# Kernel tuning notes

Measured on AMD Instinct MI355X. Metric: run time of the kernel, lower is better.

The kernel has to match this reference:

```python
import jax, jax.numpy as jnp
import numpy as np

NUM_SUBSET = 3
BN_EPS = 1e-5


def setup_inputs() -> dict:
    key = jax.random.key(0)
    ks = jax.random.split(key, 6)
    N, C, T, V = 32, 192, 256, 25
    x = jax.random.normal(ks[0], (N, C, T, V), dtype=jnp.float32)
    w_in = jax.random.normal(ks[1], (3 * C, C), dtype=jnp.float32) * (1.0 / np.sqrt(C))
    b_in = jax.random.normal(ks[2], (3 * C,), dtype=jnp.float32) * 0.02
    w_ff = jax.random.normal(ks[3], (C, C), dtype=jnp.float32) * (1.0 / np.sqrt(C))
    b_ff = jax.random.normal(ks[4], (C,), dtype=jnp.float32) * 0.02
    bn_gamma = jnp.ones((C,), dtype=jnp.float32)
    bn_beta = jnp.zeros((C,), dtype=jnp.float32)
    bn_mean = jnp.zeros((C,), dtype=jnp.float32)
    bn_var = jnp.ones((C,), dtype=jnp.float32)
    return dict(x=x, w_in=w_in, b_in=b_in, w_ff=w_ff, b_ff=b_ff,
                bn_gamma=bn_gamma, bn_beta=bn_beta, bn_mean=bn_mean, bn_var=bn_var)


def reference(x, w_in, b_in, w_ff, b_ff, bn_gamma, bn_beta, bn_mean, bn_var):
    N, C, T, V = x.shape
    S = NUM_SUBSET
    mid = C // S
    # 1x1 conv QKV projection: (N,C,T,V) x (3C,C) -> (N,3C,T,V)
    qkv = jnp.einsum('nctv,dc->ndtv', x, w_in) + b_in[None, :, None, None]
    qkv = qkv.reshape(N, 3 * S, mid, T, V)
    q, k, v = jnp.split(qkv, 3, axis=1)  # each (N,S,mid,T,V)
    # tanh-normalized attention over time: (N,S,T,T)
    att = jnp.tanh(jnp.einsum('nsctv,nscqv->nstq', q, k) / (mid * V))
    y = jnp.einsum('nstq,nscqv->nsctv', att, v).reshape(N, C, T, V)
    # ff_nett: 1x1 conv + BatchNorm (inference form)
    y = jnp.einsum('nctv,dc->ndtv', y, w_ff) + b_ff[None, :, None, None]
    inv = bn_gamma / jnp.sqrt(bn_var + BN_EPS)
    y = (y - bn_mean[None, :, None, None]) * inv[None, :, None, None] + bn_beta[None, :, None, None]
    # residual + LeakyReLU(0.1)
    z = x + y
    return jnp.where(z >= 0, z, 0.1 * z)
```

## Files before the change

kernel.cpp:

```cpp
#include <hip/hip_runtime.h>

#define TV 6400
#define NCH 192
#define D3 576

typedef unsigned short u16;
typedef unsigned int   u32;

typedef __attribute__((ext_vector_type(8))) short bf16x8;
typedef __attribute__((ext_vector_type(4))) float f32x4;

__device__ __forceinline__ float bf2f(u32 h) { return __uint_as_float(h << 16); }
__device__ __forceinline__ u16 f2bf(float f) {
    u32 u = __float_as_uint(f);
    return (u16)((u + 0x7FFFu + ((u >> 16) & 1u)) >> 16);
}

__global__ __launch_bounds__(256) void k_wcast(const float* __restrict__ w_in,
                                               const float* __restrict__ w_ff,
                                               u32* __restrict__ wb) {
    int i = blockIdx.x * 256 + threadIdx.x;
    float2 f;
    if (i < 55296) f = *(const float2*)(w_in + 2 * i);
    else           f = *(const float2*)(w_ff + 2 * (i - 55296));
    wb[i] = (u32)f2bf(f.x) | ((u32)f2bf(f.y) << 16);
}

__global__ __launch_bounds__(256) void k_qkv(const float* __restrict__ x,
                                             const u16* __restrict__ w_inb,
                                             const float* __restrict__ b_in,
                                             u16* __restrict__ qkv,
                                             u16* __restrict__ qt,
                                             u16* __restrict__ kt) {
    const int p0 = blockIdx.x * 64, n = blockIdx.y;
    const int tid = threadIdx.x;
    const int wid = tid >> 6, lane = tid & 63;
    const int wd = wid & 1, wp = wid >> 1;
    const int ml = lane & 15, kq = lane >> 4;

    __shared__ __align__(16) char Bs[64 * 384];
    __shared__ __align__(16) char As[64 * 384];
    float* L = (float*)As;

    for (int cc = 0; cc < 3; ++cc) {
        const float* xn = x + ((size_t)n * NCH + cc * 64) * TV + p0;
#pragma unroll
        for (int r = 0; r < 4; ++r) {
            int idx = tid + 256 * r;
            int c = idx >> 4, p4 = idx & 15;
            float4 v = *(const float4*)(xn + (size_t)c * TV + p4 * 4);
            *(float4*)&L[c * 65 + p4 * 4] = v;
        }
        __syncthreads();
        {
            int p = tid >> 2, cq = tid & 3;
            u32 buf[8];
#pragma unroll
            for (int j = 0; j < 8; ++j) {
                float f0 = L[(cq * 16 + 2 * j) * 65 + p];
                float f1 = L[(cq * 16 + 2 * j + 1) * 65 + p];
                buf[j] = (u32)f2bf(f0) | ((u32)f2bf(f1) << 16);
            }
#pragma unroll
            for (int h = 0; h < 2; ++h) {
                int g = cc * 8 + cq * 2 + h;
                uint4 u;
                u.x = buf[h * 4]; u.y = buf[h * 4 + 1];
                u.z = buf[h * 4 + 2]; u.w = buf[h * 4 + 3];
                *(uint4*)(Bs + p * 384 + (((g & ~7) | ((g ^ p) & 7)) << 4)) = u;
            }
        }
        __syncthreads();
    }

    for (int dt = 0; dt < 9; ++dt) {
#pragma unroll
        for (int r = 0; r < 6; ++r) {
            int idx = tid + 256 * r;
            int row = idx / 24, g = idx - row * 24;
            uint4 v = *(const uint4*)(w_inb + (size_t)(dt * 64 + row) * 192 + g * 8);
            *(uint4*)(As + row * 384 + (((g & ~7) | ((g ^ row) & 7)) << 4)) = v;
        }
        __syncthreads();

        f32x4 acc[2][2];
#pragma unroll
        for (int i = 0; i < 2; i++)
#pragma unroll
            for (int j = 0; j < 2; j++)
#pragma unroll
                for (int r = 0; r < 4; r++) acc[i][j][r] = 0.f;

#pragma unroll
        for (int kk = 0; kk < 3; ++kk)
#pragma unroll
            for (int ks = 0; ks < 2; ++ks) {
                int g = kk * 8 + ks * 4 + kq;
                bf16x8 aw[2], bx[2];
#pragma unroll
                for (int mt = 0; mt < 2; ++mt) {
                    int row = wd * 32 + mt * 16 + ml;
                    aw[mt] = *(const bf16x8*)(As + row * 384 + (((g & ~7) | ((g ^ row) & 7)) << 4));
                }
#pragma unroll
                for (int nt = 0; nt < 2; ++nt) {
                    int row = wp * 32 + nt * 16 + ml;
                    bx[nt] = *(const bf16x8*)(Bs + row * 384 + (((g & ~7) | ((g ^ row) & 7)) << 4));
                }
#pragma unroll
                for (int mt = 0; mt < 2; ++mt)
#pragma unroll
                    for (int nt = 0; nt < 2; ++nt)
                        acc[mt][nt] = __builtin_amdgcn_mfma_f32_16x16x32_bf16(aw[mt], bx[nt], acc[mt][nt], 0, 0, 0);
            }

        if (dt < 6) {
            const int s = (dt < 3) ? dt : dt - 3;
            u16* dstb = (dt < 3 ? qt : kt) + ((size_t)(n * 3 + s) * 6400 + p0) * 64;
#pragma unroll
            for (int mt = 0; mt < 2; ++mt) {
                int c = wd * 32 + mt * 16 + kq * 4;
                float4 bias = *(const float4*)(b_in + dt * 64 + c);
#pragma unroll
                for (int nt = 0; nt < 2; ++nt) {
                    int p = wp * 32 + nt * 16 + ml;
                    u32 w0 = (u32)f2bf(acc[mt][nt][0] + bias.x) | ((u32)f2bf(acc[mt][nt][1] + bias.y) << 16);
                    u32 w1 = (u32)f2bf(acc[mt][nt][2] + bias.z) | ((u32)f2bf(acc[mt][nt][3] + bias.w) << 16);
                    uint2 u; u.x = w0; u.y = w1;
                    *(uint2*)(dstb + (size_t)p * 64 + c) = u;
                }
            }
        } else {
#pragma unroll
            for (int mt = 0; mt < 2; ++mt) {
                int d = dt * 64 + wd * 32 + mt * 16 + kq * 4;
                float4 bias = *(const float4*)(b_in + d);
                u16* vdst = qkv + ((size_t)n * D3 + d) * TV;
#pragma unroll
                for (int nt = 0; nt < 2; ++nt) {
                    int p = p0 + wp * 32 + nt * 16 + ml;
                    vdst[(size_t)0 * TV + p] = f2bf(acc[mt][nt][0] + bias.x);
                    vdst[(size_t)1 * TV + p] = f2bf(acc[mt][nt][1] + bias.y);
                    vdst[(size_t)2 * TV + p] = f2bf(acc[mt][nt][2] + bias.z);
                    vdst[(size_t)3 * TV + p] = f2bf(acc[mt][nt][3] + bias.w);
                }
            }
        }
        __syncthreads();
    }
}

__global__ __launch_bounds__(256) void k_scores(const u16* __restrict__ qt,
                                                const u16* __restrict__ kt,
                                                u16* __restrict__ att) {
    const int b = blockIdx.z, t0 = blockIdx.y * 128, q0 = blockIdx.x * 128;
    const int tid = threadIdx.x;
    const int wid = tid >> 6, lane = tid & 63;
    const int wm = wid & 1, wn = wid >> 1;
    const int ml = lane & 15, kq = lane >> 4;

    __shared__ __align__(16) char As[128 * 128];
    __shared__ __align__(16) char Bs[128 * 128];

    f32x4 acc[4][4];
#pragma unroll
    for (int i = 0; i < 4; i++)
#pragma unroll
        for (int j = 0; j < 4; j++)
#pragma unroll
            for (int r = 0; r < 4; r++) acc[i][j][r] = 0.f;

    const u16* qb = qt + (size_t)b * 256 * 1600;
    const u16* kb = kt + (size_t)b * 256 * 1600;

    for (int kc = 0; kc < 1600; kc += 64) {
#pragma unroll
        for (int r = 0; r < 4; r++) {
            int idx = tid + 256 * r;
            int row = idx >> 3, g = idx & 7;
            uint4 v = *(const uint4*)(qb + (size_t)(t0 + row) * 1600 + kc + g * 8);
            *(uint4*)(As + row * 128 + (((g ^ row) & 7) << 4)) = v;
        }
#pragma unroll
        for (int r = 0; r < 4; r++) {
            int idx = tid + 256 * r;
            int row = idx >> 3, g = idx & 7;
            uint4 v = *(const uint4*)(kb + (size_t)(q0 + row) * 1600 + kc + g * 8);
            *(uint4*)(Bs + row * 128 + (((g ^ row) & 7) << 4)) = v;
        }
        __syncthreads();
#pragma unroll
        for (int ks = 0; ks < 2; ks++) {
            int gb = ks * 4 + kq;
            bf16x8 a[4], bb[4];
#pragma unroll
            for (int mt = 0; mt < 4; mt++) {
                int row = wm * 64 + mt * 16 + ml;
                a[mt] = *(const bf16x8*)(As + row * 128 + (((gb ^ row) & 7) << 4));
            }
#pragma unroll
            for (int nt = 0; nt < 4; nt++) {
                int row = wn * 64 + nt * 16 + ml;
                bb[nt] = *(const bf16x8*)(Bs + row * 128 + (((gb ^ row) & 7) << 4));
            }
#pragma unroll
            for (int mt = 0; mt < 4; mt++)
#pragma unroll
                for (int nt = 0; nt < 4; nt++)
                    acc[mt][nt] = __builtin_amdgcn_mfma_f32_16x16x32_bf16(a[mt], bb[nt], acc[mt][nt], 0, 0, 0);
        }
        __syncthreads();
    }

    const float sc = 1.0f / 1600.0f;
    u16* ab = att + (size_t)b * 65536;
#pragma unroll
    for (int mt = 0; mt < 4; mt++)
#pragma unroll
        for (int nt = 0; nt < 4; nt++) {
            int q = q0 + wn * 64 + nt * 16 + ml;
#pragma unroll
            for (int r = 0; r < 4; r++) {
                int t = t0 + wm * 64 + mt * 16 + kq * 4 + r;
                ab[(size_t)t * 256 + q] = f2bf(tanhf(acc[mt][nt][r] * sc));
            }
        }
}

__global__ __launch_bounds__(256) void k_trv(const u16* __restrict__ qkv,
                                             u16* __restrict__ vt) {
    const int q0 = blockIdx.x * 32;
    const int c0 = blockIdx.y * 32;
    const int b  = blockIdx.z;
    const int n = b / 3, s = b % 3;
    const int tid = threadIdx.x;

    __shared__ u16 L[32 * 800];

    const u16* src = qkv + ((size_t)n * D3 + 384 + s * 64 + c0) * TV + q0 * 25;
#pragma unroll
    for (int r = 0; r < 13; ++r) {
        int idx = tid + 256 * r;
        if (idx < 3200) {
            int c = idx / 100, w = idx - 100 * c;
            uint4 v = *(const uint4*)(src + (size_t)c * TV + w * 8);
            *(uint4*)&L[c * 800 + w * 8] = v;
        }
    }
    __syncthreads();

    u16* dst = vt + ((size_t)b * 1600 + c0) * 256 + q0;
#pragma unroll
    for (int r = 0; r < 4; ++r) {
        int idx = tid + 256 * r;
        if (idx < 800) {
            int c = idx / 25, v = idx - 25 * c;
            const u16* lp = &L[c * 800 + v];
            u32 buf[16];
#pragma unroll
            for (int j = 0; j < 16; ++j) {
                u32 lo = lp[(2 * j) * 25];
                u32 hi = lp[(2 * j + 1) * 25];
                buf[j] = lo | (hi << 16);
            }
            u16* dp = dst + (size_t)(v * 64 + c) * 256;
#pragma unroll
            for (int q4 = 0; q4 < 4; ++q4) {
                uint4 u; u.x = buf[q4 * 4]; u.y = buf[q4 * 4 + 1];
                u.z = buf[q4 * 4 + 2]; u.w = buf[q4 * 4 + 3];
                *(uint4*)(dp + q4 * 8) = u;
            }
        }
    }
}

__global__ __launch_bounds__(256) void k_av(const u16* __restrict__ att,
                                            const u16* __restrict__ vt,
                                            u16* __restrict__ y_t) {
    const int b = blockIdx.z, t0 = blockIdx.y * 128, v = blockIdx.x;
    const int n = b / 3, s = b % 3;
    const int tid = threadIdx.x;
    const int wid = tid >> 6, lane = tid & 63;
    const int wm = wid & 1, wn = wid >> 1;
    const int ml = lane & 15, kq = lane >> 4;

    __shared__ __align__(16) char As[128 * 128];
    __shared__ __align__(16) char Bs[64 * 128];

    f32x4 acc[4][2];
#pragma unroll
    for (int i = 0; i < 4; i++)
#pragma unroll
        for (int j = 0; j < 2; j++)
#pragma unroll
            for (int r = 0; r < 4; r++) acc[i][j][r] = 0.f;

    const u16* ab = att + (size_t)b * 65536;
    const u16* vb = vt + ((size_t)b * 1600 + v * 64) * 256;

    for (int kc = 0; kc < 256; kc += 64) {
#pragma unroll
        for (int r = 0; r < 4; r++) {
            int idx = tid + 256 * r;
            int row = idx >> 3, g = idx & 7;
            uint4 u = *(const uint4*)(ab + (size_t)(t0 + row) * 256 + kc + g * 8);
            *(uint4*)(As + row * 128 + (((g ^ row) & 7) << 4)) = u;
        }
#pragma unroll
        for (int r = 0; r < 2; r++) {
            int idx = tid + 256 * r;
            int row = idx >> 3, g = idx & 7;
            uint4 u = *(const uint4*)(vb + (size_t)row * 256 + kc + g * 8);
            *(uint4*)(Bs + row * 128 + (((g ^ row) & 7) << 4)) = u;
        }
        __syncthreads();
#pragma unroll
        for (int ks = 0; ks < 2; ks++) {
            int gb = ks * 4 + kq;
            bf16x8 a[4], bb[2];
#pragma unroll
            for (int mt = 0; mt < 4; mt++) {
                int row = wm * 64 + mt * 16 + ml;
                a[mt] = *(const bf16x8*)(As + row * 128 + (((gb ^ row) & 7) << 4));
            }
#pragma unroll
            for (int nt = 0; nt < 2; nt++) {
                int row = wn * 32 + nt * 16 + ml;
                bb[nt] = *(const bf16x8*)(Bs + row * 128 + (((gb ^ row) & 7) << 4));
            }
#pragma unroll
            for (int mt = 0; mt < 4; mt++)
#pragma unroll
                for (int nt = 0; nt < 2; nt++)
                    acc[mt][nt] = __builtin_amdgcn_mfma_f32_16x16x32_bf16(a[mt], bb[nt], acc[mt][nt], 0, 0, 0);
        }
        __syncthreads();
    }

#pragma unroll
    for (int mt = 0; mt < 4; mt++)
#pragma unroll
        for (int nt = 0; nt < 2; nt++) {
            int cg = s * 64 + wn * 32 + nt * 16 + ml;
#pragma unroll
            for (int r = 0; r < 4; r++) {
                int t = t0 + wm * 64 + mt * 16 + kq * 4 + r;
                y_t[((size_t)n * TV + t * 25 + v) * 192 + cg] = f2bf(acc[mt][nt][r]);
            }
        }
}

__global__ __launch_bounds__(256) void k_ff(const u16* __restrict__ y_t,
                                            const float* __restrict__ x,
                                            const u16* __restrict__ w_ffb,
                                            const float* __restrict__ b_ff,
                                            const float* __restrict__ gamma,
                                            const float* __restrict__ beta,
                                            const float* __restrict__ mean,
                                            const float* __restrict__ var,
                                            float* __restrict__ out) {
    const int n = blockIdx.y, p0 = blockIdx.x * 128;
    const int tid = threadIdx.x;
    const int wid = tid >> 6, lane = tid & 63;
    const int wn = wid;
    const int ml = lane & 15, kq = lane >> 4;

    __shared__ __align__(16) char Aw[64 * 384];
    __shared__ __align__(16) char By[128 * 384];

#pragma unroll
    for (int r = 0; r < 12; ++r) {
        int idx = tid + 256 * r;
        int row = idx / 24, g = idx - row * 24;
        uint4 v = *(const uint4*)(y_t + ((size_t)n * TV + p0 + row) * 192 + g * 8);
        *(uint4*)(By + row * 384 + (((g & ~7) | ((g ^ row) & 7)) << 4)) = v;
    }

    for (int dt = 0; dt < 3; ++dt) {
#pragma unroll
        for (int r = 0; r < 6; ++r) {
            int idx = tid + 256 * r;
            int row = idx / 24, g = idx - row * 24;
            uint4 v = *(const uint4*)(w_ffb + (size_t)(dt * 64 + row) * 192 + g * 8);
            *(uint4*)(Aw + row * 384 + (((g & ~7) | ((g ^ row) & 7)) << 4)) = v;
        }
        __syncthreads();

        f32x4 acc[4][2];
#pragma unroll
        for (int i = 0; i < 4; i++)
#pragma unroll
            for (int j = 0; j < 2; j++)
#pragma unroll
                for (int r = 0; r < 4; r++) acc[i][j][r] = 0.f;

#pragma unroll
        for (int kk = 0; kk < 3; ++kk)
#pragma unroll
            for (int ks = 0; ks < 2; ++ks) {
                int g = kk * 8 + ks * 4 + kq;
                bf16x8 a[4], bb[2];
#pragma unroll
                for (int mt = 0; mt < 4; mt++) {
                    int row = mt * 16 + ml;
                    a[mt] = *(const bf16x8*)(Aw + row * 384 + (((g & ~7) | ((g ^ row) & 7)) << 4));
                }
#pragma unroll
                for (int nt = 0; nt < 2; nt++) {
                    int row = wn * 32 + nt * 16 + ml;
                    bb[nt] = *(const bf16x8*)(By + row * 384 + (((g & ~7) | ((g ^ row) & 7)) << 4));
                }
#pragma unroll
                for (int mt = 0; mt < 4; mt++)
#pragma unroll
                    for (int nt = 0; nt < 2; nt++)
                        acc[mt][nt] = __builtin_amdgcn_mfma_f32_16x16x32_bf16(a[mt], bb[nt], acc[mt][nt], 0, 0, 0);
            }

#pragma unroll
        for (int mt = 0; mt < 4; mt++)
#pragma unroll
            for (int r = 0; r < 4; r++) {
                int d = dt * 64 + mt * 16 + kq * 4 + r;
                float inv = gamma[d] * rsqrtf(var[d] + 1e-5f);
                float bias = b_ff[d], mu = mean[d], bt = beta[d];
#pragma unroll
                for (int nt = 0; nt < 2; nt++) {
                    int p = p0 + wn * 32 + nt * 16 + ml;
                    size_t xi = ((size_t)n * NCH + d) * TV + p;
                    float v = acc[mt][nt][r] + bias;
                    v = (v - mu) * inv + bt;
                    float z = x[xi] + v;
                    out[xi] = (z >= 0.f) ? z : 0.1f * z;
                }
            }
        __syncthreads();
    }
}

extern "C" void kernel_launch(void* const* d_in, const int* in_sizes, int n_in,
                              void* d_out, int out_size, void* d_ws, size_t ws_size,
                              hipStream_t stream) {
    const float* x     = (const float*)d_in[0];
    const float* w_in  = (const float*)d_in[1];
    const float* b_in  = (const float*)d_in[2];
    const float* w_ff  = (const float*)d_in[3];
    const float* b_ff  = (const float*)d_in[4];
    const float* gamma = (const float*)d_in[5];
    const float* beta  = (const float*)d_in[6];
    const float* mean  = (const float*)d_in[7];
    const float* var   = (const float*)d_in[8];

    u16* qkv = (u16*)d_ws;
    u16* att = (u16*)((char*)d_ws + 235929600ull);
    u16* y_t = (u16*)((char*)d_ws + 248512512ull);
    u32* wb  = (u32*)((char*)d_ws + 327155712ull);
    u16* w_inb = (u16*)wb;
    u16* w_ffb = w_inb + 110592;
    u16* qt = (u16*)d_out;
    u16* kt = qt + 39321600ull;
    u16* vt = qt;
    float* out = (float*)d_out;

    k_wcast <<<dim3(288),        dim3(256), 0, stream>>>(w_in, w_ff, wb);
    k_qkv   <<<dim3(100, 32),    dim3(256), 0, stream>>>(x, w_inb, b_in, qkv, qt, kt);
    k_scores<<<dim3(2, 2, 96),   dim3(256), 0, stream>>>(qt, kt, att);
    k_trv   <<<dim3(8, 2, 96),   dim3(256), 0, stream>>>(qkv, vt);
    k_av    <<<dim3(25, 2, 96),  dim3(256), 0, stream>>>(att, vt, y_t);
    k_ff    <<<dim3(50, 32),     dim3(256), 0, stream>>>(y_t, x, w_ffb, b_ff, gamma, beta, mean, var, out);
}
```

Measured before the change: 584.8 us.

## Enlarge position tiles in QKV projection and attention-value GEMM kernels

The QKV projection kernel now handles 128 positions per block instead of 64, halving the grid. It loads the weight-tile fragments into registers once per output tile and reuses them across four N-subtiles. The attention-times-V kernel now tiles over a flattened (v,c) dimension of 128 instead of one joint per block, with clamped loads and guarded stores for the ragged tail. This raises MFMA work per shared-memory load and reduces redundant attention-tile loads, at the cost of more registers and LDS and fewer blocks in flight.

```diff
diff --git a/kernel.cpp b/kernel.cpp
--- a/kernel.cpp
+++ b/kernel.cpp
@@ -32,38 +32,38 @@
                                              u16* __restrict__ qkv,
                                              u16* __restrict__ qt,
                                              u16* __restrict__ kt) {
-    const int p0 = blockIdx.x * 64, n = blockIdx.y;
+    const int p0 = blockIdx.x * 128, n = blockIdx.y;
     const int tid = threadIdx.x;
     const int wid = tid >> 6, lane = tid & 63;
     const int wd = wid & 1, wp = wid >> 1;
     const int ml = lane & 15, kq = lane >> 4;
 
-    __shared__ __align__(16) char Bs[64 * 384];
+    __shared__ __align__(16) char Bs[128 * 384];
     __shared__ __align__(16) char As[64 * 384];
     float* L = (float*)As;
 
-    for (int cc = 0; cc < 3; ++cc) {
-        const float* xn = x + ((size_t)n * NCH + cc * 64) * TV + p0;
+    for (int cc = 0; cc < 6; ++cc) {
+        const float* xn = x + ((size_t)n * NCH + cc * 32) * TV + p0;
 #pragma unroll
         for (int r = 0; r < 4; ++r) {
             int idx = tid + 256 * r;
-            int c = idx >> 4, p4 = idx & 15;
+            int c = idx >> 5, p4 = idx & 31;
             float4 v = *(const float4*)(xn + (size_t)c * TV + p4 * 4);
-            *(float4*)&L[c * 65 + p4 * 4] = v;
+            *(float4*)&L[c * 129 + p4 * 4] = v;
         }
         __syncthreads();
         {
-            int p = tid >> 2, cq = tid & 3;
+            int p = tid >> 1, half = tid & 1;
             u32 buf[8];
 #pragma unroll
             for (int j = 0; j < 8; ++j) {
-                float f0 = L[(cq * 16 + 2 * j) * 65 + p];
-                float f1 = L[(cq * 16 + 2 * j + 1) * 65 + p];
+                float f0 = L[(half * 16 + 2 * j) * 129 + p];
+                float f1 = L[(half * 16 + 2 * j + 1) * 129 + p];
                 buf[j] = (u32)f2bf(f0) | ((u32)f2bf(f1) << 16);
             }
 #pragma unroll
             for (int h = 0; h < 2; ++h) {
-                int g = cc * 8 + cq * 2 + h;
+                int g = cc * 4 + half * 2 + h;
                 uint4 u;
                 u.x = buf[h * 4]; u.y = buf[h * 4 + 1];
                 u.z = buf[h * 4 + 2]; u.w = buf[h * 4 + 3];
@@ -83,11 +83,24 @@
         }
         __syncthreads();
 
-        f32x4 acc[2][2];
+        bf16x8 aw[2][3][2];
+#pragma unroll
+        for (int mt = 0; mt < 2; ++mt) {
+            int row = wd * 32 + mt * 16 + ml;
+#pragma unroll
+            for (int kk = 0; kk < 3; ++kk)
+#pragma unroll
+                for (int ks = 0; ks < 2; ++ks) {
+                    int g = kk * 8 + ks * 4 + kq;
+                    aw[mt][kk][ks] = *(const bf16x8*)(As + row * 384 + (((g & ~7) | ((g ^ row) & 7)) << 4));
+                }
+        }
+
+        f32x4 acc[2][4];
 #pragma unroll
         for (int i = 0; i < 2; i++)
 #pragma unroll
-            for (int j = 0; j < 2; j++)
+            for (int j = 0; j < 4; j++)
 #pragma unroll
                 for (int r = 0; r < 4; r++) acc[i][j][r] = 0.f;
 
@@ -96,22 +109,17 @@
 #pragma unroll
             for (int ks = 0; ks < 2; ++ks) {
                 int g = kk * 8 + ks * 4 + kq;
-                bf16x8 aw[2], bx[2];
-#pragma unroll
-                for (int mt = 0; mt < 2; ++mt) {
-                    int row = wd * 32 + mt * 16 + ml;
-                    aw[mt] = *(const bf16x8*)(As + row * 384 + (((g & ~7) | ((g ^ row) & 7)) << 4));
-                }
-#pragma unroll
-                for (int nt = 0; nt < 2; ++nt) {
-                    int row = wp * 32 + nt * 16 + ml;
+                bf16x8 bx[4];
+#pragma unroll
+                for (int nt = 0; nt < 4; ++nt) {
+                    int row = wp * 64 + nt * 16 + ml;
                     bx[nt] = *(const bf16x8*)(Bs + row * 384 + (((g & ~7) | ((g ^ row) & 7)) << 4));
                 }
 #pragma unroll
                 for (int mt = 0; mt < 2; ++mt)
 #pragma unroll
-                    for (int nt = 0; nt < 2; ++nt)
-                        acc[mt][nt] = __builtin_amdgcn_mfma_f32_16x16x32_bf16(aw[mt], bx[nt], acc[mt][nt], 0, 0, 0);
+                    for (int nt = 0; nt < 4; ++nt)
+                        acc[mt][nt] = __builtin_amdgcn_mfma_f32_16x16x32_bf16(aw[mt][kk][ks], bx[nt], acc[mt][nt], 0, 0, 0);
             }
 
         if (dt < 6) {
@@ -122,8 +130,8 @@
                 int c = wd * 32 + mt * 16 + kq * 4;
                 float4 bias = *(const float4*)(b_in + dt * 64 + c);
 #pragma unroll
-                for (int nt = 0; nt < 2; ++nt) {
-                    int p = wp * 32 + nt * 16 + ml;
+                for (int nt = 0; nt < 4; ++nt) {
+                    int p = wp * 64 + nt * 16 + ml;
                     u32 w0 = (u32)f2bf(acc[mt][nt][0] + bias.x) | ((u32)f2bf(acc[mt][nt][1] + bias.y) << 16);
                     u32 w1 = (u32)f2bf(acc[mt][nt][2] + bias.z) | ((u32)f2bf(acc[mt][nt][3] + bias.w) << 16);
                     uint2 u; u.x = w0; u.y = w1;
@@ -137,8 +145,8 @@
                 float4 bias = *(const float4*)(b_in + d);
                 u16* vdst = qkv + ((size_t)n * D3 + d) * TV;
 #pragma unroll
-                for (int nt = 0; nt < 2; ++nt) {
-                    int p = p0 + wp * 32 + nt * 16 + ml;
+                for (int nt = 0; nt < 4; ++nt) {
+                    int p = p0 + wp * 64 + nt * 16 + ml;
                     vdst[(size_t)0 * TV + p] = f2bf(acc[mt][nt][0] + bias.x);
                     vdst[(size_t)1 * TV + p] = f2bf(acc[mt][nt][1] + bias.y);
                     vdst[(size_t)2 * TV + p] = f2bf(acc[mt][nt][2] + bias.z);
@@ -277,7 +285,7 @@
 __global__ __launch_bounds__(256) void k_av(const u16* __restrict__ att,
                                             const u16* __restrict__ vt,
                                             u16* __restrict__ y_t) {
-    const int b = blockIdx.z, t0 = blockIdx.y * 128, v = blockIdx.x;
+    const int b = blockIdx.z, t0 = blockIdx.y * 128, cv0 = blockIdx.x * 128;
     const int n = b / 3, s = b % 3;
     const int tid = threadIdx.x;
     const int wid = tid >> 6, lane = tid & 63;
@@ -285,18 +293,18 @@
     const int ml = lane & 15, kq = lane >> 4;
 
     __shared__ __align__(16) char As[128 * 128];
-    __shared__ __align__(16) char Bs[64 * 128];
-
-    f32x4 acc[4][2];
+    __shared__ __align__(16) char Bs[128 * 128];
+
+    f32x4 acc[4][4];
 #pragma unroll
     for (int i = 0; i < 4; i++)
 #pragma unroll
-        for (int j = 0; j < 2; j++)
+        for (int j = 0; j < 4; j++)
 #pragma unroll
             for (int r = 0; r < 4; r++) acc[i][j][r] = 0.f;
 
     const u16* ab = att + (size_t)b * 65536;
-    const u16* vb = vt + ((size_t)b * 1600 + v * 64) * 256;
+    const u16* vb = vt + (size_t)b * 1600 * 256;
 
     for (int kc = 0; kc < 256; kc += 64) {
 #pragma unroll
@@ -307,31 +315,32 @@
             *(uint4*)(As + row * 128 + (((g ^ row) & 7) << 4)) = u;
         }
 #pragma unroll
-        for (int r = 0; r < 2; r++) {
+        for (int r = 0; r < 4; r++) {
             int idx = tid + 256 * r;
             int row = idx >> 3, g = idx & 7;
-            uint4 u = *(const uint4*)(vb + (size_t)row * 256 + kc + g * 8);
+            int gr = cv0 + row; if (gr > 1599) gr = 1599;
+            uint4 u = *(const uint4*)(vb + (size_t)gr * 256 + kc + g * 8);
             *(uint4*)(Bs + row * 128 + (((g ^ row) & 7) << 4)) = u;
         }
         __syncthreads();
 #pragma unroll
         for (int ks = 0; ks < 2; ks++) {
             int gb = ks * 4 + kq;
-            bf16x8 a[4], bb[2];
+            bf16x8 a[4], bb[4];
 #pragma unroll
             for (int mt = 0; mt < 4; mt++) {
                 int row = wm * 64 + mt * 16 + ml;
                 a[mt] = *(const bf16x8*)(As + row * 128 + (((gb ^ row) & 7) << 4));
             }
 #pragma unroll
-            for (int nt = 0; nt < 2; nt++) {
-                int row = wn * 32 + nt * 16 + ml;
+            for (int nt = 0; nt < 4; nt++) {
+                int row = wn * 64 + nt * 16 + ml;
                 bb[nt] = *(const bf16x8*)(Bs + row * 128 + (((gb ^ row) & 7) << 4));
             }
 #pragma unroll
             for (int mt = 0; mt < 4; mt++)
 #pragma unroll
-                for (int nt = 0; nt < 2; nt++)
+                for (int nt = 0; nt < 4; nt++)
                     acc[mt][nt] = __builtin_amdgcn_mfma_f32_16x16x32_bf16(a[mt], bb[nt], acc[mt][nt], 0, 0, 0);
         }
         __syncthreads();
@@ -340,12 +349,16 @@
 #pragma unroll
     for (int mt = 0; mt < 4; mt++)
 #pragma unroll
-        for (int nt = 0; nt < 2; nt++) {
-            int cg = s * 64 + wn * 32 + nt * 16 + ml;
-#pragma unroll
-            for (int r = 0; r < 4; r++) {
-                int t = t0 + wm * 64 + mt * 16 + kq * 4 + r;
-                y_t[((size_t)n * TV + t * 25 + v) * 192 + cg] = f2bf(acc[mt][nt][r]);
+        for (int nt = 0; nt < 4; nt++) {
+            int cv = cv0 + wn * 64 + nt * 16 + ml;
+            if (cv < 1600) {
+                int v = cv >> 6, c = cv & 63;
+                int cg = s * 64 + c;
+#pragma unroll
+                for (int r = 0; r < 4; r++) {
+                    int t = t0 + wm * 64 + mt * 16 + kq * 4 + r;
+                    y_t[((size_t)n * TV + t * 25 + v) * 192 + cg] = f2bf(acc[mt][nt][r]);
+                }
             }
         }
 }
@@ -463,9 +476,9 @@
     float* out = (float*)d_out;
 
     k_wcast <<<dim3(288),        dim3(256), 0, stream>>>(w_in, w_ff, wb);
-    k_qkv   <<<dim3(100, 32),    dim3(256), 0, stream>>>(x, w_inb, b_in, qkv, qt, kt);
+    k_qkv   <<<dim3(50, 32),     dim3(256), 0, stream>>>(x, w_inb, b_in, qkv, qt, kt);
     k_scores<<<dim3(2, 2, 96),   dim3(256), 0, stream>>>(qt, kt, att);
     k_trv   <<<dim3(8, 2, 96),   dim3(256), 0, stream>>>(qkv, vt);
-    k_av    <<<dim3(25, 2, 96),  dim3(256), 0, stream>>>(att, vt, y_t);
+    k_av    <<<dim3(13, 2, 96),  dim3(256), 0, stream>>>(att, vt, y_t);
     k_ff    <<<dim3(50, 32),     dim3(256), 0, stream>>>(y_t, x, w_ffb, b_ff, gamma, beta, mean, var, out);
 }
```

Result: slower. 600.6 us (+2.7%).

## Pre-swizzle weight images and prefetch weight tiles into LDS via global_load_lds

Applied to the files above, without the earlier changes.

The weight cast kernel now writes bf16 weights already laid out in the XOR-swizzled LDS tile order, so k_qkv and k_ff can copy each 24 KB tile straight into shared memory with direct global-to-LDS 16-byte loads. The next weight tile's load is issued right after the MFMA loop, so it overlaps the epilogue stores. This removes the register round trip and per-element address swizzling on weight loads. The cost is relying on correct synchronization for the async LDS writes, which only reach LDS after a wait.

```diff
diff --git a/kernel.cpp b/kernel.cpp
--- a/kernel.cpp
+++ b/kernel.cpp
@@ -9,6 +9,12 @@
 
 typedef __attribute__((ext_vector_type(8))) short bf16x8;
 typedef __attribute__((ext_vector_type(4))) float f32x4;
+
+typedef const __attribute__((address_space(1))) void gvoid;
+typedef __attribute__((address_space(3))) void lvoid;
+__device__ __forceinline__ void gload16(gvoid* g, lvoid* l) {
+    __builtin_amdgcn_global_load_lds(g, l, 16, 0, 0);
+}
 
 __device__ __forceinline__ float bf2f(u32 h) { return __uint_as_float(h << 16); }
 __device__ __forceinline__ u16 f2bf(float f) {
@@ -20,14 +26,19 @@
                                                const float* __restrict__ w_ff,
                                                u32* __restrict__ wb) {
     int i = blockIdx.x * 256 + threadIdx.x;
-    float2 f;
-    if (i < 55296) f = *(const float2*)(w_in + 2 * i);
-    else           f = *(const float2*)(w_ff + 2 * (i - 55296));
+    int j; const float* ws;
+    if (i < 55296) { j = i;         ws = w_in; }
+    else           { j = i - 55296; ws = w_ff; }
+    int tile = j / 6144, rem = j - tile * 6144;
+    int row = rem / 96,  rb  = rem - row * 96;
+    int slot = rb >> 2,  e   = rb & 3;
+    int g = (slot & ~7) | ((slot ^ row) & 7);
+    float2 f = *(const float2*)(ws + (tile * 64 + row) * 192 + g * 8 + e * 2);
     wb[i] = (u32)f2bf(f.x) | ((u32)f2bf(f.y) << 16);
 }
 
 __global__ __launch_bounds__(256) void k_qkv(const float* __restrict__ x,
-                                             const u16* __restrict__ w_inb,
+                                             const u16* __restrict__ w_img,
                                              const float* __restrict__ b_in,
                                              u16* __restrict__ qkv,
                                              u16* __restrict__ qt,
@@ -73,14 +84,15 @@
         __syncthreads();
     }
 
+    const char* wsrc = (const char*)w_img;
+
+#pragma unroll
+    for (int r = 0; r < 6; ++r) {
+        int off = (tid + 256 * r) * 16;
+        gload16((gvoid*)(wsrc + off), (lvoid*)(As + off));
+    }
+
     for (int dt = 0; dt < 9; ++dt) {
-#pragma unroll
-        for (int r = 0; r < 6; ++r) {
-            int idx = tid + 256 * r;
-            int row = idx / 24, g = idx - row * 24;
-            uint4 v = *(const uint4*)(w_inb + (size_t)(dt * 64 + row) * 192 + g * 8);
-            *(uint4*)(As + row * 384 + (((g & ~7) | ((g ^ row) & 7)) << 4)) = v;
-        }
         __syncthreads();
 
         f32x4 acc[2][2];
@@ -113,6 +125,16 @@
                     for (int nt = 0; nt < 2; ++nt)
                         acc[mt][nt] = __builtin_amdgcn_mfma_f32_16x16x32_bf16(aw[mt], bx[nt], acc[mt][nt], 0, 0, 0);
             }
+
+        __syncthreads();
+
+        if (dt < 8) {
+#pragma unroll
+            for (int r = 0; r < 6; ++r) {
+                int off = (tid + 256 * r) * 16;
+                gload16((gvoid*)(wsrc + (size_t)(dt + 1) * 24576 + off), (lvoid*)(As + off));
+            }
+        }
 
         if (dt < 6) {
             const int s = (dt < 3) ? dt : dt - 3;
@@ -146,7 +168,6 @@
                 }
             }
         }
-        __syncthreads();
     }
 }
 
@@ -352,7 +373,7 @@
 
 __global__ __launch_bounds__(256) void k_ff(const u16* __restrict__ y_t,
                                             const float* __restrict__ x,
-                                            const u16* __restrict__ w_ffb,
+                                            const u16* __restrict__ wff_img,
                                             const float* __restrict__ b_ff,
                                             const float* __restrict__ gamma,
                                             const float* __restrict__ beta,
@@ -368,6 +389,14 @@
     __shared__ __align__(16) char Aw[64 * 384];
     __shared__ __align__(16) char By[128 * 384];
 
+    const char* wsrc = (const char*)wff_img;
+
+#pragma unroll
+    for (int r = 0; r < 6; ++r) {
+        int off = (tid + 256 * r) * 16;
+        gload16((gvoid*)(wsrc + off), (lvoid*)(Aw + off));
+    }
+
 #pragma unroll
     for (int r = 0; r < 12; ++r) {
         int idx = tid + 256 * r;
@@ -377,13 +406,6 @@
     }
 
     for (int dt = 0; dt < 3; ++dt) {
-#pragma unroll
-        for (int r = 0; r < 6; ++r) {
-            int idx = tid + 256 * r;
-            int row = idx / 24, g = idx - row * 24;
-            uint4 v = *(const uint4*)(w_ffb + (size_t)(dt * 64 + row) * 192 + g * 8);
-            *(uint4*)(Aw + row * 384 + (((g & ~7) | ((g ^ row) & 7)) << 4)) = v;
-        }
         __syncthreads();
 
         f32x4 acc[4][2];
@@ -416,6 +438,16 @@
                     for (int nt = 0; nt < 2; nt++)
                         acc[mt][nt] = __builtin_amdgcn_mfma_f32_16x16x32_bf16(a[mt], bb[nt], acc[mt][nt], 0, 0, 0);
             }
+
+        __syncthreads();
+
+        if (dt < 2) {
+#pragma unroll
+            for (int r = 0; r < 6; ++r) {
+                int off = (tid + 256 * r) * 16;
+                gload16((gvoid*)(wsrc + (size_t)(dt + 1) * 24576 + off), (lvoid*)(Aw + off));
+            }
+        }
 
 #pragma unroll
         for (int mt = 0; mt < 4; mt++)
@@ -434,7 +466,6 @@
                     out[xi] = (z >= 0.f) ? z : 0.1f * z;
                 }
             }
-        __syncthreads();
     }
 }
 
@@ -455,17 +486,17 @@
     u16* att = (u16*)((char*)d_ws + 235929600ull);
     u16* y_t = (u16*)((char*)d_ws + 248512512ull);
     u32* wb  = (u32*)((char*)d_ws + 327155712ull);
-    u16* w_inb = (u16*)wb;
-    u16* w_ffb = w_inb + 110592;
+    u16* w_img   = (u16*)wb;
+    u16* wff_img = w_img + 110592;
     u16* qt = (u16*)d_out;
     u16* kt = qt + 39321600ull;
     u16* vt = qt;
     float* out = (float*)d_out;
 
     k_wcast <<<dim3(288),        dim3(256), 0, stream>>>(w_in, w_ff, wb);
-    k_qkv   <<<dim3(100, 32),    dim3(256), 0, stream>>>(x, w_inb, b_in, qkv, qt, kt);
+    k_qkv   <<<dim3(100, 32),    dim3(256), 0, stream>>>(x, w_img, b_in, qkv, qt, kt);
     k_scores<<<dim3(2, 2, 96),   dim3(256), 0, stream>>>(qt, kt, att);
     k_trv   <<<dim3(8, 2, 96),   dim3(256), 0, stream>>>(qkv, vt);
     k_av    <<<dim3(25, 2, 96),  dim3(256), 0, stream>>>(att, vt, y_t);
-    k_ff    <<<dim3(50, 32),     dim3(256), 0, stream>>>(y_t, x, w_ffb, b_ff, gamma, beta, mean, var, out);
-}
+    k_ff    <<<dim3(50, 32),     dim3(256), 0, stream>>>(y_t, x, wff_img, b_ff, gamma, beta, mean, var, out);
+}
```

Result: no change. 594.0 us (+1.6%).
